# Kernel tuning notes

Measured on AMD Instinct MI355X. Metric: run time of the kernel, lower is better.

Reference implementation:

```python
import jax, jax.numpy as jnp
import numpy as np

B, F, D, L, N = 2048, 40, 64, 3, 40  # batch, num_fields, embed_dim, num_layers, num_subspaces


def setup_inputs() -> dict:
    key = jax.random.key(0)
    inputs = jax.random.normal(key, (B, F, D), dtype=jnp.float32)
    # Parameters per layer, matching torch init exactly:
    #   W     = identity(D) repeated over out_subspaces -> [N, D, D]
    #   alpha = ones([num_fields, in_subspaces, out_subspaces]); in_subspaces == F for
    #           layer 0 and == N afterwards; with N == F all layers share shape [F, N, N]
    #   h     = ones([N, D, 1])
    W = jnp.broadcast_to(jnp.eye(D, dtype=jnp.float32), (L, N, D, D)).copy()
    alpha = jnp.ones((L, F, N, N), dtype=jnp.float32)
    h = jnp.ones((L, N, D, 1), dtype=jnp.float32)
    return {"inputs": inputs, "W": W, "alpha": alpha, "h": h}


def _fusion_layer(B0, Bi, W, alpha, h):
    # Original math: fusion[b,n,D,d] = sum_{f,i} alpha[f,i,n] * B0[b,f,D] * Bi[b,i,d]
    #                out[b,n,D]     = sum_d fusion[b,n,D,d] * W[n,D,d] * h[n,d]
    # Reordered to avoid the [b,f,n,D,d] outer-product tensor:
    M = W * h[:, :, 0][:, None, :]                 # [n, D, d] = W * h broadcast over D
    C = jnp.einsum('bid,nDd->binD', Bi, M)         # contract embed dim d first
    out = jnp.einsum('bfD,fin,binD->bnD', B0, alpha, C)
    return out


def reference(inputs, W, alpha, h):
    B_i = inputs
    for l in range(L):
        B_i = _fusion_layer(inputs, B_i, W[l], alpha[l], h[l])
    return B_i
```

## Files before the change

kernel.cpp:

```cpp
#include <hip/hip_runtime.h>


typedef __bf16 bf16x8 __attribute__((ext_vector_type(8)));
typedef float  f32x16 __attribute__((ext_vector_type(16)));

constexpr int BATCH = 2048;
constexpr int FDIM  = 40;
constexpr int DDIM  = 64;
constexpr int LAY   = 3;
constexpr int IPAD  = 64;
constexpr int FPAD  = 48;
constexpr int NHALF = 20;
constexpr int MB_BYTES  = DDIM * DDIM * 2;
constexpr int AT_BYTES  = IPAD * FPAD * 2;
constexpr int BUF_BYTES = MB_BYTES + AT_BYTES;

__device__ __forceinline__ unsigned short f2bf(float f) {
  union { float f; unsigned u; } v; v.f = f;
  unsigned r = v.u + 0x7fff + ((v.u >> 16) & 1);
  return (unsigned short)(r >> 16);
}

__device__ __forceinline__ void async16(const void* g, void* l) {
  __builtin_amdgcn_global_load_lds(
      (const __attribute__((address_space(1))) unsigned int*)g,
      (__attribute__((address_space(3))) unsigned int*)l, 16, 0, 0);
}

__global__ void prep_k(const float* __restrict__ W, const float* __restrict__ h,
                       const float* __restrict__ alpha, const float* __restrict__ inputs,
                       unsigned short* __restrict__ M, unsigned short* __restrict__ AT,
                       unsigned short* __restrict__ B0b, unsigned short* __restrict__ B0T) {
  int i = blockIdx.x * blockDim.x + threadIdx.x;
  const int nM  = LAY * FDIM * DDIM * DDIM;
  const int nAT = LAY * FDIM * IPAD * FPAD;
  const int nB  = BATCH * FDIM * DDIM;
  const int nT  = BATCH * DDIM * FPAD;
  if (i < nM) {
    int d  = i & 63;
    int ln = i >> 12;
    M[i] = f2bf(W[i] * h[ln * DDIM + d]);
    return;
  }
  i -= nM;
  if (i < nAT) {
    int f  = i % FPAD;
    int ii = (i / FPAD) % IPAD;
    int n  = (i / (FPAD * IPAD)) % FDIM;
    int l  = i / (FPAD * IPAD * FDIM);
    float v = 0.f;
    if (f < FDIM && ii < FDIM)
      v = alpha[(((size_t)l * FDIM + f) * FDIM + ii) * FDIM + n];
    AT[i] = f2bf(v);
    return;
  }
  i -= nAT;
  if (i < nB) { B0b[i] = f2bf(inputs[i]); return; }
  i -= nB;
  if (i >= nT) return;
  int b   = i / (DDIM * FPAD);
  int rem = i - b * (DDIM * FPAD);
  int d   = rem / FPAD;
  int f   = rem - d * FPAD;
  B0T[i] = (f < FDIM) ? f2bf(inputs[((size_t)b * FDIM + f) * DDIM + d]) : (unsigned short)0;
}

template <bool FINAL>
__global__ __launch_bounds__(128, 2) void layer_k(
    const unsigned short* __restrict__ Bi,
    const unsigned short* __restrict__ B0T,
    const unsigned short* __restrict__ Mt,
    const unsigned short* __restrict__ ATt,
    void* __restrict__ outp)
{
  __shared__ __align__(16) unsigned short smem[2 * BUF_BYTES / 2];

  const int tid  = threadIdx.x;
  const int lane = tid & 63;
  const int w    = tid >> 6;
  const int c    = lane & 31;
  const int h    = lane >> 5;
  const int bg   = blockIdx.x >> 1;
  const int nBase = (blockIdx.x & 1) * NHALF;
  const int bb   = bg * 4 + w * 2;

  auto stage = [&](int n, int buf) {
    const unsigned short* Mn = Mt  + n * (DDIM * DDIM);
    const unsigned short* An = ATt + n * (IPAD * FPAD);
    char* base = (char*)smem + buf * BUF_BYTES;
#pragma unroll
    for (int r = 0; r < 4; ++r) {
      int p  = r * 128 + tid;
      int D  = p >> 3, pc = p & 7;
      int cd = pc ^ (D & 7);
      async16(Mn + D * DDIM + cd * 8, base + r * 2048 + w * 1024);
    }
#pragma unroll
    for (int r = 0; r < 3; ++r)
      async16(An + r * 1024 + tid * 8, base + MB_BYTES + r * 2048 + w * 1024);
  };

  bf16x8 aBi[2][2][4];
#pragma unroll
  for (int b2 = 0; b2 < 2; ++b2)
#pragma unroll
    for (int it = 0; it < 2; ++it) {
      int row = it * 32 + c; if (row > FDIM - 1) row = FDIM - 1;
#pragma unroll
      for (int ks = 0; ks < 4; ++ks)
        aBi[b2][it][ks] = *reinterpret_cast<const bf16x8*>(
            Bi + ((size_t)(bb + b2) * FDIM + row) * DDIM + ks * 16 + h * 8);
    }

  bf16x8 bT[2][2][3];
#pragma unroll
  for (int b2 = 0; b2 < 2; ++b2)
#pragma unroll
    for (int dt = 0; dt < 2; ++dt)
#pragma unroll
      for (int ks = 0; ks < 3; ++ks)
        bT[b2][dt][ks] = *reinterpret_cast<const bf16x8*>(
            B0T + ((size_t)(bb + b2) * DDIM + dt * 32 + c) * FPAD + ks * 16 + h * 8);

  stage(nBase, 0);

  for (int ln = 0; ln < NHALF; ++ln) {
    const int n = nBase + ln;
    __syncthreads();
    const int buf = ln & 1;
    if (ln + 1 < NHALF) stage(n + 1, buf ^ 1);

    const char* bufp = (const char*)smem + buf * BUF_BYTES;

    bf16x8 mb[2][4];
#pragma unroll
    for (int dt = 0; dt < 2; ++dt)
#pragma unroll
      for (int ks = 0; ks < 4; ++ks) {
        int pc = (ks * 2 + h) ^ (c & 7);
        mb[dt][ks] = *reinterpret_cast<const bf16x8*>(
            bufp + (dt * 32 + c) * 128 + pc * 16);
      }

    float pout[2][2] = {{0.f, 0.f}, {0.f, 0.f}};

#pragma unroll
    for (int it = 0; it < 2; ++it) {
      bf16x8 at[3];
#pragma unroll
      for (int ks = 0; ks < 3; ++ks)
        at[ks] = *reinterpret_cast<const bf16x8*>(
            bufp + MB_BYTES + ((it * 32 + c) * FPAD + ks * 16 + h * 8) * 2);

#pragma unroll
      for (int dt = 0; dt < 2; ++dt) {
        f32x16 aC0 = {0,0,0,0,0,0,0,0,0,0,0,0,0,0,0,0};
        f32x16 aC1 = {0,0,0,0,0,0,0,0,0,0,0,0,0,0,0,0};
        f32x16 aR0 = {0,0,0,0,0,0,0,0,0,0,0,0,0,0,0,0};
        f32x16 aR1 = {0,0,0,0,0,0,0,0,0,0,0,0,0,0,0,0};
#pragma unroll
        for (int ks = 0; ks < 4; ++ks) {
          aC0 = __builtin_amdgcn_mfma_f32_32x32x16_bf16(aBi[0][it][ks], mb[dt][ks], aC0, 0, 0, 0);
          aC1 = __builtin_amdgcn_mfma_f32_32x32x16_bf16(aBi[1][it][ks], mb[dt][ks], aC1, 0, 0, 0);
        }
#pragma unroll
        for (int ks = 0; ks < 3; ++ks) {
          aR0 = __builtin_amdgcn_mfma_f32_32x32x16_bf16(at[ks], bT[0][dt][ks], aR0, 0, 0, 0);
          aR1 = __builtin_amdgcn_mfma_f32_32x32x16_bf16(at[ks], bT[1][dt][ks], aR1, 0, 0, 0);
        }
        {
          float t0 = 0.f, t1 = 0.f, t2 = 0.f, t3 = 0.f;
#pragma unroll
          for (int r = 0; r < 4; ++r) {
            t0 += aC0[r] * aR0[r];       t1 += aC0[r + 4] * aR0[r + 4];
            t2 += aC0[r + 8] * aR0[r + 8]; t3 += aC0[r + 12] * aR0[r + 12];
          }
          pout[0][dt] += (t0 + t1) + (t2 + t3);
        }
        {
          float t0 = 0.f, t1 = 0.f, t2 = 0.f, t3 = 0.f;
#pragma unroll
          for (int r = 0; r < 4; ++r) {
            t0 += aC1[r] * aR1[r];       t1 += aC1[r + 4] * aR1[r + 4];
            t2 += aC1[r + 8] * aR1[r + 8]; t3 += aC1[r + 12] * aR1[r + 12];
          }
          pout[1][dt] += (t0 + t1) + (t2 + t3);
        }
      }
    }

#pragma unroll
    for (int b2 = 0; b2 < 2; ++b2) {
      float v0 = pout[b2][0] + __shfl_xor(pout[b2][0], 32, 64);
      float v1 = pout[b2][1] + __shfl_xor(pout[b2][1], 32, 64);
      float val = h ? v1 : v0;
      size_t off = ((size_t)(bb + b2) * FDIM + n) * DDIM + lane;
      if (FINAL) ((float*)outp)[off] = val;
      else       ((unsigned short*)outp)[off] = f2bf(val);
    }
  }
}

extern "C" void kernel_launch(void* const* d_in, const int* in_sizes, int n_in,
                              void* d_out, int out_size, void* d_ws, size_t ws_size,
                              hipStream_t stream) {
  const float* inputs = (const float*)d_in[0];
  const float* W      = (const float*)d_in[1];
  const float* alpha  = (const float*)d_in[2];
  const float* h      = (const float*)d_in[3];

  char* ws = (char*)d_ws;
  const size_t S   = (size_t)BATCH * FDIM * DDIM * 2;
  const size_t ST  = (size_t)BATCH * DDIM * FPAD * 2;
  unsigned short* Bi1 = (unsigned short*)(ws);
  unsigned short* Bi2 = (unsigned short*)(ws + S);
  unsigned short* B0b = (unsigned short*)(ws + 2 * S);
  unsigned short* B0T = (unsigned short*)(ws + 3 * S);
  unsigned short* Mb  = (unsigned short*)(ws + 3 * S + ST);
  unsigned short* ATb = (unsigned short*)(ws + 3 * S + ST + (size_t)LAY * FDIM * DDIM * DDIM * 2);

  const int nPrep = LAY * FDIM * DDIM * DDIM + LAY * FDIM * IPAD * FPAD
                  + BATCH * FDIM * DDIM + BATCH * DDIM * FPAD;
  prep_k<<<(nPrep + 255) / 256, 256, 0, stream>>>(W, h, alpha, inputs, Mb, ATb, B0b, B0T);

  dim3 grid(BATCH / 4 * 2), blk(128);
  const size_t mL = (size_t)FDIM * DDIM * DDIM;
  const size_t aL = (size_t)FDIM * IPAD * FPAD;
  layer_k<false><<<grid, blk, 0, stream>>>(B0b, B0T, Mb, ATb, Bi1);
  layer_k<false><<<grid, blk, 0, stream>>>(Bi1, B0T, Mb + mL, ATb + aL, Bi2);
  layer_k<true ><<<grid, blk, 0, stream>>>(Bi2, B0T, Mb + 2 * mL, ATb + 2 * aL, d_out);
}
```

Measured before the change: 268.5 us.

## Split work per wave by batch and D-tile, each block covering all fields

Reorganizes layer_k so that each 256-thread block handles 2 batch rows over all 40 output subspaces. Each wave now owns one (batch, D-tile) pair instead of 2 batches × 2 D-tiles over half the subspaces. This cuts per-thread register state (fewer accumulators and operand fragments) so more waves fit per CU, and it halves redundant per-block loads of Bi/B0T. In exchange, every block streams all 40 M/alpha tiles, doubling LDS staging traffic per batch pair, and only half of the lanes write outputs.

```diff
diff --git a/kernel.cpp b/kernel.cpp
--- a/kernel.cpp
+++ b/kernel.cpp
@@ -10,7 +10,6 @@
 constexpr int LAY   = 3;
 constexpr int IPAD  = 64;
 constexpr int FPAD  = 48;
-constexpr int NHALF = 20;
 constexpr int MB_BYTES  = DDIM * DDIM * 2;
 constexpr int AT_BYTES  = IPAD * FPAD * 2;
 constexpr int BUF_BYTES = MB_BYTES + AT_BYTES;
@@ -66,7 +65,7 @@
 }
 
 template <bool FINAL>
-__global__ __launch_bounds__(128, 2) void layer_k(
+__global__ __launch_bounds__(256, 4) void layer_k(
     const unsigned short* __restrict__ Bi,
     const unsigned short* __restrict__ B0T,
     const unsigned short* __restrict__ Mt,
@@ -78,72 +77,62 @@
   const int tid  = threadIdx.x;
   const int lane = tid & 63;
   const int w    = tid >> 6;
+  const int b2   = w >> 1;
+  const int dt   = w & 1;
   const int c    = lane & 31;
   const int h    = lane >> 5;
-  const int bg   = blockIdx.x >> 1;
-  const int nBase = (blockIdx.x & 1) * NHALF;
-  const int bb   = bg * 4 + w * 2;
+  const int b    = blockIdx.x * 2 + b2;
 
   auto stage = [&](int n, int buf) {
     const unsigned short* Mn = Mt  + n * (DDIM * DDIM);
     const unsigned short* An = ATt + n * (IPAD * FPAD);
     char* base = (char*)smem + buf * BUF_BYTES;
 #pragma unroll
-    for (int r = 0; r < 4; ++r) {
-      int p  = r * 128 + tid;
+    for (int r = 0; r < 2; ++r) {
+      int p  = r * 256 + tid;
       int D  = p >> 3, pc = p & 7;
       int cd = pc ^ (D & 7);
-      async16(Mn + D * DDIM + cd * 8, base + r * 2048 + w * 1024);
+      async16(Mn + D * DDIM + cd * 8, base + r * 4096 + w * 1024);
     }
-#pragma unroll
-    for (int r = 0; r < 3; ++r)
-      async16(An + r * 1024 + tid * 8, base + MB_BYTES + r * 2048 + w * 1024);
+    async16(An + tid * 8, base + MB_BYTES + w * 1024);
+    if (w < 2)
+      async16(An + (256 + tid) * 8, base + MB_BYTES + 4096 + w * 1024);
   };
 
-  bf16x8 aBi[2][2][4];
+  bf16x8 aBi[2][4];
 #pragma unroll
-  for (int b2 = 0; b2 < 2; ++b2)
+  for (int it = 0; it < 2; ++it) {
+    int row = it * 32 + c; if (row > FDIM - 1) row = FDIM - 1;
 #pragma unroll
-    for (int it = 0; it < 2; ++it) {
-      int row = it * 32 + c; if (row > FDIM - 1) row = FDIM - 1;
+    for (int ks = 0; ks < 4; ++ks)
+      aBi[it][ks] = *reinterpret_cast<const bf16x8*>(
+          Bi + ((size_t)b * FDIM + row) * DDIM + ks * 16 + h * 8);
+  }
+
+  bf16x8 bT[3];
 #pragma unroll
-      for (int ks = 0; ks < 4; ++ks)
-        aBi[b2][it][ks] = *reinterpret_cast<const bf16x8*>(
-            Bi + ((size_t)(bb + b2) * FDIM + row) * DDIM + ks * 16 + h * 8);
-    }
+  for (int ks = 0; ks < 3; ++ks)
+    bT[ks] = *reinterpret_cast<const bf16x8*>(
+        B0T + ((size_t)b * DDIM + dt * 32 + c) * FPAD + ks * 16 + h * 8);
 
-  bf16x8 bT[2][2][3];
-#pragma unroll
-  for (int b2 = 0; b2 < 2; ++b2)
-#pragma unroll
-    for (int dt = 0; dt < 2; ++dt)
-#pragma unroll
-      for (int ks = 0; ks < 3; ++ks)
-        bT[b2][dt][ks] = *reinterpret_cast<const bf16x8*>(
-            B0T + ((size_t)(bb + b2) * DDIM + dt * 32 + c) * FPAD + ks * 16 + h * 8);
+  stage(0, 0);
 
-  stage(nBase, 0);
-
-  for (int ln = 0; ln < NHALF; ++ln) {
-    const int n = nBase + ln;
+  for (int n = 0; n < FDIM; ++n) {
     __syncthreads();
-    const int buf = ln & 1;
-    if (ln + 1 < NHALF) stage(n + 1, buf ^ 1);
+    const int buf = n & 1;
+    if (n + 1 < FDIM) stage(n + 1, buf ^ 1);
 
     const char* bufp = (const char*)smem + buf * BUF_BYTES;
 
-    bf16x8 mb[2][4];
+    bf16x8 mb[4];
 #pragma unroll
-    for (int dt = 0; dt < 2; ++dt)
-#pragma unroll
-      for (int ks = 0; ks < 4; ++ks) {
-        int pc = (ks * 2 + h) ^ (c & 7);
-        mb[dt][ks] = *reinterpret_cast<const bf16x8*>(
-            bufp + (dt * 32 + c) * 128 + pc * 16);
-      }
+    for (int ks = 0; ks < 4; ++ks) {
+      int D  = dt * 32 + c;
+      int pc = (ks * 2 + h) ^ (D & 7);
+      mb[ks] = *reinterpret_cast<const bf16x8*>(bufp + D * 128 + pc * 16);
+    }
 
-    float pout[2][2] = {{0.f, 0.f}, {0.f, 0.f}};
-
+    float pout = 0.f;
 #pragma unroll
     for (int it = 0; it < 2; ++it) {
       bf16x8 at[3];
@@ -152,51 +141,29 @@
         at[ks] = *reinterpret_cast<const bf16x8*>(
             bufp + MB_BYTES + ((it * 32 + c) * FPAD + ks * 16 + h * 8) * 2);
 
+      f32x16 aC = {0,0,0,0,0,0,0,0,0,0,0,0,0,0,0,0};
+      f32x16 aR = {0,0,0,0,0,0,0,0,0,0,0,0,0,0,0,0};
 #pragma unroll
-      for (int dt = 0; dt < 2; ++dt) {
-        f32x16 aC0 = {0,0,0,0,0,0,0,0,0,0,0,0,0,0,0,0};
-        f32x16 aC1 = {0,0,0,0,0,0,0,0,0,0,0,0,0,0,0,0};
-        f32x16 aR0 = {0,0,0,0,0,0,0,0,0,0,0,0,0,0,0,0};
-        f32x16 aR1 = {0,0,0,0,0,0,0,0,0,0,0,0,0,0,0,0};
+      for (int ks = 0; ks < 4; ++ks)
+        aC = __builtin_amdgcn_mfma_f32_32x32x16_bf16(aBi[it][ks], mb[ks], aC, 0, 0, 0);
 #pragma unroll
-        for (int ks = 0; ks < 4; ++ks) {
-          aC0 = __builtin_amdgcn_mfma_f32_32x32x16_bf16(aBi[0][it][ks], mb[dt][ks], aC0, 0, 0, 0);
-          aC1 = __builtin_amdgcn_mfma_f32_32x32x16_bf16(aBi[1][it][ks], mb[dt][ks], aC1, 0, 0, 0);
-        }
+      for (int ks = 0; ks < 3; ++ks)
+        aR = __builtin_amdgcn_mfma_f32_32x32x16_bf16(at[ks], bT[ks], aR, 0, 0, 0);
+
+      float t0 = 0.f, t1 = 0.f, t2 = 0.f, t3 = 0.f;
 #pragma unroll
-        for (int ks = 0; ks < 3; ++ks) {
-          aR0 = __builtin_amdgcn_mfma_f32_32x32x16_bf16(at[ks], bT[0][dt][ks], aR0, 0, 0, 0);
-          aR1 = __builtin_amdgcn_mfma_f32_32x32x16_bf16(at[ks], bT[1][dt][ks], aR1, 0, 0, 0);
-        }
-        {
-          float t0 = 0.f, t1 = 0.f, t2 = 0.f, t3 = 0.f;
-#pragma unroll
-          for (int r = 0; r < 4; ++r) {
-            t0 += aC0[r] * aR0[r];       t1 += aC0[r + 4] * aR0[r + 4];
-            t2 += aC0[r + 8] * aR0[r + 8]; t3 += aC0[r + 12] * aR0[r + 12];
-          }
-          pout[0][dt] += (t0 + t1) + (t2 + t3);
-        }
-        {
-          float t0 = 0.f, t1 = 0.f, t2 = 0.f, t3 = 0.f;
-#pragma unroll
-          for (int r = 0; r < 4; ++r) {
-            t0 += aC1[r] * aR1[r];       t1 += aC1[r + 4] * aR1[r + 4];
-            t2 += aC1[r + 8] * aR1[r + 8]; t3 += aC1[r + 12] * aR1[r + 12];
-          }
-          pout[1][dt] += (t0 + t1) + (t2 + t3);
-        }
+      for (int r = 0; r < 4; ++r) {
+        t0 += aC[r] * aR[r];         t1 += aC[r + 4] * aR[r + 4];
+        t2 += aC[r + 8] * aR[r + 8]; t3 += aC[r + 12] * aR[r + 12];
       }
+      pout += (t0 + t1) + (t2 + t3);
     }
 
-#pragma unroll
-    for (int b2 = 0; b2 < 2; ++b2) {
-      float v0 = pout[b2][0] + __shfl_xor(pout[b2][0], 32, 64);
-      float v1 = pout[b2][1] + __shfl_xor(pout[b2][1], 32, 64);
-      float val = h ? v1 : v0;
-      size_t off = ((size_t)(bb + b2) * FDIM + n) * DDIM + lane;
-      if (FINAL) ((float*)outp)[off] = val;
-      else       ((unsigned short*)outp)[off] = f2bf(val);
+    float v = pout + __shfl_xor(pout, 32, 64);
+    if (lane < 32) {
+      size_t off = ((size_t)b * FDIM + n) * DDIM + dt * 32 + lane;
+      if (FINAL) ((float*)outp)[off] = v;
+      else       ((unsigned short*)outp)[off] = f2bf(v);
     }
   }
 }
@@ -223,7 +190,7 @@
                   + BATCH * FDIM * DDIM + BATCH * DDIM * FPAD;
   prep_k<<<(nPrep + 255) / 256, 256, 0, stream>>>(W, h, alpha, inputs, Mb, ATb, B0b, B0T);
 
-  dim3 grid(BATCH / 4 * 2), blk(128);
+  dim3 grid(BATCH / 2), blk(256);
   const size_t mL = (size_t)FDIM * DDIM * DDIM;
   const size_t aL = (size_t)FDIM * IPAD * FPAD;
   layer_k<false><<<grid, blk, 0, stream>>>(B0b, B0T, Mb, ATb, Bi1);
```

Result: slower. 292.7 us (+9.0%).
